# Kernel optimization log

Measured on AMD Instinct MI355X. Metric: run time of the kernel, lower is better.

The kernel has to match this reference:

```python
import jax, jax.numpy as jnp
import numpy as np

EMB = 768
HEADS = 12
HD = EMB // HEADS
DFF = 4 * EMB
EPS = 1e-5


def layernorm(x, g, b):
    mu = jnp.mean(x, axis=-1, keepdims=True)
    var = jnp.mean(jnp.square(x - mu), axis=-1, keepdims=True)
    return (x - mu) * jax.lax.rsqrt(var + EPS) * g + b


def setup_inputs() -> dict:
    key = jax.random.key(0)
    ks = jax.random.split(key, 12)
    B, L = 16, 1024
    std = 0.02
    return {
        "x": jax.random.normal(ks[0], (B, L, EMB), jnp.float32),
        "ln1_g": jnp.ones((EMB,), jnp.float32),
        "ln1_b": jnp.zeros((EMB,), jnp.float32),
        "Wq": jax.random.normal(ks[1], (EMB, EMB), jnp.float32) * std,
        "bq": jnp.zeros((EMB,), jnp.float32),
        "Wk": jax.random.normal(ks[2], (EMB, EMB), jnp.float32) * std,
        "bk": jnp.zeros((EMB,), jnp.float32),
        "Wv": jax.random.normal(ks[3], (EMB, EMB), jnp.float32) * std,
        "bv": jnp.zeros((EMB,), jnp.float32),
        "Wo": jax.random.normal(ks[4], (EMB, EMB), jnp.float32) * std,
        "bo": jnp.zeros((EMB,), jnp.float32),
        "ln2_g": jnp.ones((EMB,), jnp.float32),
        "ln2_b": jnp.zeros((EMB,), jnp.float32),
        "W1": jax.random.normal(ks[5], (EMB, DFF), jnp.float32) * std,
        "b1": jnp.zeros((DFF,), jnp.float32),
        "W2": jax.random.normal(ks[6], (DFF, EMB), jnp.float32) * std,
        "b2": jnp.zeros((EMB,), jnp.float32),
    }


def reference(x, ln1_g, ln1_b, Wq, bq, Wk, bk, Wv, bv, Wo, bo,
              ln2_g, ln2_b, W1, b1, W2, b2):
    B, L, D = x.shape
    # --- attention (pre-LN) ---
    h = layernorm(x, ln1_g, ln1_b)
    q = (h @ Wq + bq).reshape(B, L, HEADS, HD)
    k = (h @ Wk + bk).reshape(B, L, HEADS, HD)
    v = (h @ Wv + bv).reshape(B, L, HEADS, HD)
    scores = jnp.einsum("blhd,bmhd->bhlm", q, k) / np.sqrt(HD).astype(np.float32)
    attn = jax.nn.softmax(scores, axis=-1)
    ctx = jnp.einsum("bhlm,bmhd->blhd", attn, v).reshape(B, L, D)
    x = x + ctx @ Wo + bo
    # --- MLP (pre-LN), dropout is identity in eval ---
    h = layernorm(x, ln2_g, ln2_b)
    h = jax.nn.gelu(h @ W1 + b1, approximate=False)  # torch nn.GELU default = exact erf
    x = x + h @ W2 + b2
    return x
```

## Files before the change

kernel.cpp:

```cpp
#include <hip/hip_runtime.h>
#include <hip/hip_bf16.h>
#include <math.h>

#define EMB 768
#define DFF 3072
#define HEADS 12
#define HD 64
#define LSEQ 1024
#define BATCH 16
#define BL (BATCH * LSEQ)
#define QKVD 2304
#define QSCALE 0.1803368801111204f

typedef __attribute__((ext_vector_type(8))) short short8;
typedef __attribute__((ext_vector_type(4))) float floatx4;
typedef unsigned short u16;

__device__ __forceinline__ u16 f2bf(float f) {
  union { float f; unsigned u; } c; c.f = f;
  unsigned u = c.u;
  u += 0x7fffu + ((u >> 16) & 1u);
  return (u16)(u >> 16);
}
__device__ __forceinline__ u16 f2bf_trunc(float f) {
  union { float f; unsigned u; } c; c.f = f;
  return (u16)(c.u >> 16);
}
__device__ __forceinline__ float fast_exp2(float x) {
#if __has_builtin(__builtin_amdgcn_exp2f)
  return __builtin_amdgcn_exp2f(x);
#else
  return exp2f(x);
#endif
}
__device__ __forceinline__ float fast_rcp(float x) {
#if __has_builtin(__builtin_amdgcn_rcpf)
  return __builtin_amdgcn_rcpf(x);
#else
  return 1.0f / x;
#endif
}
__device__ __forceinline__ float gelu_fast(float x) {
  float x2 = x * x;
  float u = x * fmaf(0.10294540f, x2, 2.30211423f);
  u = fminf(fmaxf(u, -30.f), 30.f);
  float t = fast_exp2(u);
  return x * t * fast_rcp(t + 1.0f);
}
__device__ __forceinline__ void async16(const u16* g, u16* l) {
  __builtin_amdgcn_global_load_lds(
      (const __attribute__((address_space(1))) unsigned int*)g,
      (__attribute__((address_space(3))) unsigned int*)l, 16, 0, 0);
}
__device__ __forceinline__ short8 load16(const u16* p) {
  return *reinterpret_cast<const short8*>(p);
}

__global__ __launch_bounds__(256) void ln_kernel(const float* __restrict__ x,
                                                 const float* __restrict__ g,
                                                 const float* __restrict__ b,
                                                 u16* __restrict__ out) {
  int row = blockIdx.x * 4 + (threadIdx.x >> 6);
  int lane = threadIdx.x & 63;
  const float* xr = x + (size_t)row * EMB;
  float v[12];
#pragma unroll
  for (int i = 0; i < 3; i++) {
    float4 t = *reinterpret_cast<const float4*>(xr + i * 256 + lane * 4);
    v[i*4+0] = t.x; v[i*4+1] = t.y; v[i*4+2] = t.z; v[i*4+3] = t.w;
  }
  float s = 0.f, ss = 0.f;
#pragma unroll
  for (int i = 0; i < 12; i++) { s += v[i]; ss += v[i] * v[i]; }
#pragma unroll
  for (int off = 1; off < 64; off <<= 1) {
    s  += __shfl_xor(s, off);
    ss += __shfl_xor(ss, off);
  }
  float mu  = s * (1.f / 768.f);
  float var = ss * (1.f / 768.f) - mu * mu;
  float rs  = rsqrtf(var + 1e-5f);
  u16* orow = out + (size_t)row * EMB;
#pragma unroll
  for (int i = 0; i < 3; i++) {
    int col = i * 256 + lane * 4;
    ushort4 o;
    o.x = f2bf((v[i*4+0] - mu) * rs * g[col+0] + b[col+0]);
    o.y = f2bf((v[i*4+1] - mu) * rs * g[col+1] + b[col+1]);
    o.z = f2bf((v[i*4+2] - mu) * rs * g[col+2] + b[col+2]);
    o.w = f2bf((v[i*4+3] - mu) * rs * g[col+3] + b[col+3]);
    *reinterpret_cast<ushort4*>(orow + col) = o;
  }
}

__global__ void prep_kernel(const float* __restrict__ Wq, const float* __restrict__ Wk,
                            const float* __restrict__ Wv, const float* __restrict__ Wo,
                            const float* __restrict__ W1, const float* __restrict__ W2,
                            u16* __restrict__ wqkv, u16* __restrict__ wot,
                            u16* __restrict__ w1t, u16* __restrict__ w2t,
                            const float* __restrict__ bq, const float* __restrict__ bk,
                            const float* __restrict__ bv, float* __restrict__ obias) {
  __shared__ float t[32][33];
  int id = blockIdx.x;
  int tx = threadIdx.x, ty = threadIdx.y;
  if (id >= 6912) {
    int i = (id - 6912) * 256 + ty * 32 + tx;
    if (i < QKVD)
      obias[i] = i < EMB ? bq[i] : (i < 2*EMB ? bk[i - EMB] : bv[i - 2*EMB]);
    return;
  }
  const float* in; u16* out; int K, N, bx, by;
  if (id < 2304) {
    int seg = id / 576, rem = id % 576;
    bx = rem % 24; by = rem / 24; K = EMB; N = EMB;
    in = seg == 0 ? Wq : seg == 1 ? Wk : seg == 2 ? Wv : Wo;
    out = seg == 3 ? wot : wqkv + (size_t)seg * EMB * EMB;
  } else if (id < 4608) {
    int rem = id - 2304; bx = rem % 96; by = rem / 96;
    in = W1; out = w1t; K = EMB; N = DFF;
  } else {
    int rem = id - 4608; bx = rem % 24; by = rem / 24;
    in = W2; out = w2t; K = DFF; N = EMB;
  }
  int x0 = bx * 32, y0 = by * 32;
#pragma unroll
  for (int i = 0; i < 4; i++)
    t[ty + i*8][tx] = in[(size_t)(y0 + ty + i*8) * N + x0 + tx];
  __syncthreads();
#pragma unroll
  for (int i = 0; i < 4; i++)
    out[(size_t)(x0 + ty + i*8) * K + y0 + tx] = f2bf(t[tx][ty + i*8]);
}

__global__ void vtrans_kernel(const u16* __restrict__ qkv, u16* __restrict__ vt) {
  __shared__ u16 t[32][33];
  int l0 = blockIdx.x * 32;
  int d0 = blockIdx.y * 32;
  int bh = blockIdx.z;
  int b = bh / HEADS, h = bh % HEADS;
  int tx = threadIdx.x, ty = threadIdx.y;
#pragma unroll
  for (int i = 0; i < 4; i++)
    t[ty + i*8][tx] = qkv[(size_t)(b * LSEQ + l0 + ty + i*8) * QKVD + 2*EMB + h * HD + d0 + tx];
  __syncthreads();
#pragma unroll
  for (int i = 0; i < 4; i++)
    vt[(size_t)(bh * HD + d0 + ty + i*8) * LSEQ + l0 + tx] = t[tx][ty + i*8];
}

#define BK 64
__global__ __launch_bounds__(256) void gemm_kernel(
    const u16* __restrict__ A, const u16* __restrict__ Bt,
    const float* __restrict__ bias, const float* __restrict__ res,
    u16* __restrict__ outb, float* __restrict__ outf,
    int M, int N, int K, int mode, float scale, int scale_n) {
  __shared__ u16 As[128 * BK];
  __shared__ u16 Bs[128 * BK];
  int tid = threadIdx.x;
  int lane = tid & 63, wave = tid >> 6;
  int wm = wave & 1, wn = wave >> 1;
  int l16 = lane & 15, lhi = lane >> 4;
  int m0 = blockIdx.x * 128, n0 = blockIdx.y * 128;

  floatx4 acc[4][4];
#pragma unroll
  for (int i = 0; i < 4; i++)
#pragma unroll
    for (int j = 0; j < 4; j++) acc[i][j] = {0.f, 0.f, 0.f, 0.f};

  int rr = lane >> 3;
  int cs = ((lane & 7) ^ rr) * 8;
  const u16* aptr = A + (size_t)(m0 + wave * 32 + rr) * K + cs;
  const u16* bptr = Bt + (size_t)(n0 + wave * 32 + rr) * K + cs;
  u16* asl = As + (wave * 32) * BK;
  u16* bsl = Bs + (wave * 32) * BK;

  int l7 = l16 & 7;
  int oa0 = (wm * 64 + l16) * BK + ((lhi ^ l7) * 8);
  int ob0 = (wn * 64 + l16) * BK + ((lhi ^ l7) * 8);
  int oa1 = oa0 ^ 32;
  int ob1 = ob0 ^ 32;

  for (int k0 = 0; k0 < K; k0 += BK) {
    __syncthreads();
#pragma unroll
    for (int i = 0; i < 4; i++) {
      async16(aptr + (size_t)(i * 8) * K + k0, asl + i * 8 * BK);
      async16(bptr + (size_t)(i * 8) * K + k0, bsl + i * 8 * BK);
    }
    __syncthreads();
#pragma unroll
    for (int kk = 0; kk < 2; kk++) {
      int oA = kk ? oa1 : oa0;
      int oB = kk ? ob1 : ob0;
      short8 af[4], bfr[4];
#pragma unroll
      for (int mt = 0; mt < 4; mt++)
        af[mt] = *reinterpret_cast<const short8*>(&As[oA + mt * 16 * BK]);
#pragma unroll
      for (int nt = 0; nt < 4; nt++)
        bfr[nt] = *reinterpret_cast<const short8*>(&Bs[oB + nt * 16 * BK]);
#pragma unroll
      for (int mt = 0; mt < 4; mt++)
#pragma unroll
        for (int nt = 0; nt < 4; nt++)
          acc[mt][nt] = __builtin_amdgcn_mfma_f32_16x16x32_bf16(bfr[nt], af[mt],
                                                                acc[mt][nt], 0, 0, 0);
    }
  }

#pragma unroll
  for (int mt = 0; mt < 4; mt++) {
    int m = m0 + wm*64 + mt*16 + l16;
#pragma unroll
    for (int nt = 0; nt < 4; nt++) {
      int nbase = n0 + wn*64 + nt*16 + lhi*4;
      float4 bv = *reinterpret_cast<const float4*>(&bias[nbase]);
      float v0 = acc[mt][nt][0] + bv.x, v1 = acc[mt][nt][1] + bv.y;
      float v2 = acc[mt][nt][2] + bv.z, v3 = acc[mt][nt][3] + bv.w;
      if (mode == 1) {
        float4 r = *reinterpret_cast<const float4*>(&res[(size_t)m * N + nbase]);
        float4 o; o.x = v0 + r.x; o.y = v1 + r.y; o.z = v2 + r.z; o.w = v3 + r.w;
        *reinterpret_cast<float4*>(&outf[(size_t)m * N + nbase]) = o;
      } else {
        if (mode == 2) {
          v0 = gelu_fast(v0); v1 = gelu_fast(v1);
          v2 = gelu_fast(v2); v3 = gelu_fast(v3);
        } else {
          float sc = (nbase < scale_n) ? scale : 1.0f;
          v0 *= sc; v1 *= sc; v2 *= sc; v3 *= sc;
        }
        ushort4 o;
        o.x = f2bf(v0); o.y = f2bf(v1); o.z = f2bf(v2); o.w = f2bf(v3);
        *reinterpret_cast<ushort4*>(&outb[(size_t)m * N + nbase]) = o;
      }
    }
  }
}

#define PSTRIDE 76
__global__ __launch_bounds__(256) void flash_kernel(
    const u16* __restrict__ qkv, const u16* __restrict__ vt,
    u16* __restrict__ ctx) {
  __shared__ u16 Ps[4][2][16][PSTRIDE];
  int tid = threadIdx.x;
  int lane = tid & 63, w = tid >> 6;
  int l16 = lane & 15, lhi = lane >> 4;

  int i = blockIdx.x;
  int bh = (i & 7) | ((i >> 5) << 3);
  int qb = (i >> 3) & 3;
  int b = bh / HEADS, h = bh % HEADS;
  int q0 = qb * 256 + w * 64;

  const u16* qbase = qkv + (size_t)(b * LSEQ) * QKVD + h * HD;
  const u16* kbase = qbase + EMB;
  const u16* vbase = vt + (size_t)(bh * HD) * LSEQ;

  short8 qf[4][2];
#pragma unroll
  for (int st = 0; st < 4; st++)
#pragma unroll
    for (int kk = 0; kk < 2; kk++)
      qf[st][kk] = load16(qbase + (size_t)(q0 + st*16 + l16) * QKVD + kk*32 + lhi*8);

  floatx4 o[4][4];
#pragma unroll
  for (int st = 0; st < 4; st++)
#pragma unroll
    for (int mt = 0; mt < 4; mt++) o[st][mt] = {0.f, 0.f, 0.f, 0.f};
  float l_i[4] = {0.f, 0.f, 0.f, 0.f};

  for (int kt = 0; kt < LSEQ; kt += 64) {
    short8 kf[4][2], vf[4][2];
#pragma unroll
    for (int mt = 0; mt < 4; mt++)
#pragma unroll
      for (int kk = 0; kk < 2; kk++) {
        kf[mt][kk] = load16(kbase + (size_t)(kt + mt*16 + l16) * QKVD + kk*32 + lhi*8);
        vf[mt][kk] = load16(vbase + (size_t)(mt*16 + l16) * LSEQ + kt + kk*32 + lhi*8);
      }

#pragma unroll
    for (int st = 0; st < 4; st++) {
      u16* pbuf = &Ps[w][st & 1][0][0];
      floatx4 s[4];
#pragma unroll
      for (int mt = 0; mt < 4; mt++) s[mt] = {0.f, 0.f, 0.f, 0.f};
#pragma unroll
      for (int mt = 0; mt < 4; mt++)
#pragma unroll
        for (int kk = 0; kk < 2; kk++)
          s[mt] = __builtin_amdgcn_mfma_f32_16x16x32_bf16(kf[mt][kk], qf[st][kk],
                                                          s[mt], 0, 0, 0);
      float ls = 0.f;
#pragma unroll
      for (int mt = 0; mt < 4; mt++) {
        ushort4 pw;
        float p0 = fast_exp2(s[mt][0]), p1 = fast_exp2(s[mt][1]);
        float p2 = fast_exp2(s[mt][2]), p3 = fast_exp2(s[mt][3]);
        ls += (p0 + p1) + (p2 + p3);
        pw.x = f2bf_trunc(p0); pw.y = f2bf_trunc(p1);
        pw.z = f2bf_trunc(p2); pw.w = f2bf_trunc(p3);
        *reinterpret_cast<ushort4*>(&pbuf[l16 * PSTRIDE + mt*16 + lhi*4]) = pw;
      }
      l_i[st] += ls;
      short8 pf0 = load16(&pbuf[l16 * PSTRIDE + 0*32 + lhi*8]);
      short8 pf1 = load16(&pbuf[l16 * PSTRIDE + 1*32 + lhi*8]);
#pragma unroll
      for (int mt = 0; mt < 4; mt++) {
        o[st][mt] = __builtin_amdgcn_mfma_f32_16x16x32_bf16(vf[mt][0], pf0,
                                                            o[st][mt], 0, 0, 0);
        o[st][mt] = __builtin_amdgcn_mfma_f32_16x16x32_bf16(vf[mt][1], pf1,
                                                            o[st][mt], 0, 0, 0);
      }
    }
  }

#pragma unroll
  for (int st = 0; st < 4; st++) {
    l_i[st] += __shfl_xor(l_i[st], 16);
    l_i[st] += __shfl_xor(l_i[st], 32);
  }

#pragma unroll
  for (int st = 0; st < 4; st++) {
    float inv = fast_rcp(l_i[st]);
    size_t rowbase = (size_t)(b * LSEQ + q0 + st*16 + l16) * EMB + h * HD;
#pragma unroll
    for (int mt = 0; mt < 4; mt++) {
      ushort4 ow;
      ow.x = f2bf(o[st][mt][0] * inv); ow.y = f2bf(o[st][mt][1] * inv);
      ow.z = f2bf(o[st][mt][2] * inv); ow.w = f2bf(o[st][mt][3] * inv);
      *reinterpret_cast<ushort4*>(&ctx[rowbase + mt*16 + lhi*4]) = ow;
    }
  }
}

extern "C" void kernel_launch(void* const* d_in, const int* in_sizes, int n_in,
                              void* d_out, int out_size, void* d_ws, size_t ws_size,
                              hipStream_t stream) {
  const float* x    = (const float*)d_in[0];
  const float* ln1g = (const float*)d_in[1];
  const float* ln1b = (const float*)d_in[2];
  const float* Wq   = (const float*)d_in[3];
  const float* bq   = (const float*)d_in[4];
  const float* Wk   = (const float*)d_in[5];
  const float* bk   = (const float*)d_in[6];
  const float* Wv   = (const float*)d_in[7];
  const float* bv   = (const float*)d_in[8];
  const float* Wo   = (const float*)d_in[9];
  const float* bo   = (const float*)d_in[10];
  const float* ln2g = (const float*)d_in[11];
  const float* ln2b = (const float*)d_in[12];
  const float* W1   = (const float*)d_in[13];
  const float* b1   = (const float*)d_in[14];
  const float* W2   = (const float*)d_in[15];
  const float* b2   = (const float*)d_in[16];

  char* ws = (char*)d_ws;
  u16* qkv_bf = (u16*)(ws);
  u16* vt_bf  = (u16*)(ws + (size_t)75497472);
  u16* h_bf   = (u16*)(ws + (size_t)100663296);
  float* x2   = (float*)(ws + (size_t)125829120);
  u16* m_bf   = (u16*)(ws);
  char* wp = ws + (size_t)176160768;
  u16* wqkv = (u16*)(wp);
  u16* wot  = (u16*)(wp + (size_t)3538944);
  u16* w1t  = (u16*)(wp + (size_t)3538944 + 1179648);
  u16* w2t  = (u16*)(wp + (size_t)3538944 + 1179648 + 4718592);
  float* qkvbias = (float*)(wp + (size_t)3538944 + 1179648 + 2*4718592);

  dim3 b256(256), tb(32, 8);

  prep_kernel<<<dim3(6921), tb, 0, stream>>>(Wq, Wk, Wv, Wo, W1, W2,
      wqkv, wot, w1t, w2t, bq, bk, bv, qkvbias);

  ln_kernel<<<dim3(BL/4), b256, 0, stream>>>(x, ln1g, ln1b, h_bf);

  gemm_kernel<<<dim3(128, 18), b256, 0, stream>>>(h_bf, wqkv, qkvbias, nullptr,
      qkv_bf, nullptr, BL, QKVD, EMB, 0, QSCALE, EMB);

  vtrans_kernel<<<dim3(32, 2, BATCH*HEADS), tb, 0, stream>>>(qkv_bf, vt_bf);

  flash_kernel<<<dim3(768), b256, 0, stream>>>(qkv_bf, vt_bf, h_bf);

  gemm_kernel<<<dim3(128, 6), b256, 0, stream>>>(h_bf, wot, bo, x, nullptr, x2,
      BL, EMB, EMB, 1, 1.0f, 0);

  ln_kernel<<<dim3(BL/4), b256, 0, stream>>>(x2, ln2g, ln2b, h_bf);

  gemm_kernel<<<dim3(128, 24), b256, 0, stream>>>(h_bf, w1t, b1, nullptr, m_bf,
      nullptr, BL, DFF, EMB, 2, 1.0f, 0);

  gemm_kernel<<<dim3(128, 6), b256, 0, stream>>>(m_bf, w2t, b2, x2, nullptr,
      (float*)d_out, BL, EMB, DFF, 1, 1.0f, 0);
}
```

Baseline: 569.5 us.

## Stage K/V tiles in double-buffered swizzled LDS with async prefetch in flash kernel

Each of the four waves in a block previously loaded the full 64x64 K and V tiles from global memory into registers itself, so every tile was fetched four times. The flash kernel now loads each K and V tile once per block into shared memory with async copies, using an XOR-swizzled layout, and double-buffers them so the next tile is prefetched while the current one is processed. This cuts redundant global traffic and hides load latency, at the cost of more LDS use (lower occupancy) and a block-wide barrier on every iteration.

```diff
diff --git a/kernel.cpp b/kernel.cpp
--- a/kernel.cpp
+++ b/kernel.cpp
@@ -242,6 +242,8 @@
 __global__ __launch_bounds__(256) void flash_kernel(
     const u16* __restrict__ qkv, const u16* __restrict__ vt,
     u16* __restrict__ ctx) {
+  __shared__ u16 Kb[2][64 * 64];
+  __shared__ u16 Vb[2][64 * 64];
   __shared__ u16 Ps[4][2][16][PSTRIDE];
   int tid = threadIdx.x;
   int lane = tid & 63, w = tid >> 6;
@@ -257,6 +259,17 @@
   const u16* kbase = qbase + EMB;
   const u16* vbase = vt + (size_t)(bh * HD) * LSEQ;
 
+  int rr = lane >> 3;
+  int c8 = (lane & 7) ^ rr;
+  const u16* ksrc = kbase + (size_t)(w * 16 + rr) * QKVD + c8 * 8;
+  const u16* vsrc = vbase + (size_t)(w * 16 + rr) * LSEQ + c8 * 8;
+
+#pragma unroll
+  for (int j = 0; j < 2; j++) {
+    async16(ksrc + (size_t)(j * 8) * QKVD, &Kb[0][(w * 16 + j * 8) * 64]);
+    async16(vsrc + (size_t)(j * 8) * LSEQ, &Vb[0][(w * 16 + j * 8) * 64]);
+  }
+
   short8 qf[4][2];
 #pragma unroll
   for (int st = 0; st < 4; st++)
@@ -271,15 +284,31 @@
     for (int mt = 0; mt < 4; mt++) o[st][mt] = {0.f, 0.f, 0.f, 0.f};
   float l_i[4] = {0.f, 0.f, 0.f, 0.f};
 
+  __syncthreads();
+
+  int cur = 0;
   for (int kt = 0; kt < LSEQ; kt += 64) {
+    if (kt + 64 < LSEQ) {
+      const u16* kn = ksrc + (size_t)(kt + 64) * QKVD;
+      const u16* vn = vsrc + (kt + 64);
+#pragma unroll
+      for (int j = 0; j < 2; j++) {
+        async16(kn + (size_t)(j * 8) * QKVD, &Kb[cur ^ 1][(w * 16 + j * 8) * 64]);
+        async16(vn + (size_t)(j * 8) * LSEQ, &Vb[cur ^ 1][(w * 16 + j * 8) * 64]);
+      }
+    }
+
     short8 kf[4][2], vf[4][2];
 #pragma unroll
-    for (int mt = 0; mt < 4; mt++)
+    for (int mt = 0; mt < 4; mt++) {
+      int krow = mt * 16 + l16;
 #pragma unroll
       for (int kk = 0; kk < 2; kk++) {
-        kf[mt][kk] = load16(kbase + (size_t)(kt + mt*16 + l16) * QKVD + kk*32 + lhi*8);
-        vf[mt][kk] = load16(vbase + (size_t)(mt*16 + l16) * LSEQ + kt + kk*32 + lhi*8);
+        int slot = ((kk * 4 + lhi) ^ (krow & 7)) * 8;
+        kf[mt][kk] = load16(&Kb[cur][krow * 64 + slot]);
+        vf[mt][kk] = load16(&Vb[cur][krow * 64 + slot]);
       }
+    }
 
 #pragma unroll
     for (int st = 0; st < 4; st++) {
@@ -315,6 +344,9 @@
                                                             o[st][mt], 0, 0, 0);
       }
     }
+
+    __syncthreads();
+    cur ^= 1;
   }
 
 #pragma unroll
```

Result: no change. 566.1 us (-0.6%).
